# Kernel tuning notes

Measured on AMD Instinct MI355X. Metric: run time of the kernel, lower is better.

The kernel has to match this reference:

```python
import jax, jax.numpy as jnp
import numpy as np

B, C, H, W = 16, 256, 128, 128
RED = 16
RATES = (1, 2, 4)  # 1 + 4 + 16 = 21 pooled values per channel


def setup_inputs() -> dict:
    key = jax.random.key(0)
    ks = jax.random.split(key, 7)
    r = C // RED
    x = jax.random.normal(ks[0], (B, C, H, W), dtype=jnp.float32)
    # stacked per-channel fusion Linears: weight (C, 21), bias (C,)
    Wf = jax.random.normal(ks[1], (C, 21), dtype=jnp.float32) * 0.2
    bf = jax.random.normal(ks[2], (C,), dtype=jnp.float32) * 0.05
    # SE bottleneck FC (stored as (in, out) so y = x @ W + b)
    W1 = jax.random.normal(ks[3], (C, r), dtype=jnp.float32) * (1.0 / np.sqrt(C))
    b1 = jax.random.normal(ks[4], (r,), dtype=jnp.float32) * 0.05
    W2 = jax.random.normal(ks[5], (r, C), dtype=jnp.float32) * (1.0 / np.sqrt(r))
    b2 = jax.random.normal(ks[6], (C,), dtype=jnp.float32) * 0.05
    return {"x": x, "Wf": Wf, "bf": bf, "W1": W1, "b1": b1, "W2": W2, "b2": b2}


def _multiscale_pool(x):
    # kernel = stride = (H//rate, W//rate) -> output rate x rate, flattened
    b, c, h, w = x.shape
    outs = []
    for rate in RATES:
        ph, pw = h // rate, w // rate
        pooled = x.reshape(b, c, rate, ph, rate, pw).max(axis=(3, 5))  # (b,c,rate,rate)
        outs.append(pooled.reshape(b, c, rate * rate))
    return jnp.concatenate(outs, axis=2)  # (b, c, 21)


def reference(x, Wf, bf, W1, b1, W2, b2):
    p = _multiscale_pool(x)                              # (B, C, 21)
    fused = jnp.einsum('bcp,cp->bc', p, Wf) + bf         # per-channel 21->1 linears
    h = jax.nn.relu(fused @ W1 + b1)                      # SE squeeze
    s = h @ W2 + b2                                       # SE excite (NOTE: original forward applies NO sigmoid)
    return x * s[:, :, None, None]
```

## Files before the change

kernel.cpp:

```cpp
#include <hip/hip_runtime.h>

#define BB 16
#define CC 256
#define RR 16
#define HWPLANE 16384
#define NGROUPS 4
#define PLANES_PER_GROUP 1024

using f32x4 = __attribute__((ext_vector_type(4))) float;

__global__ __launch_bounds__(256) void pool_fuse_kernel(
    const float* __restrict__ x,
    const float* __restrict__ Wf,
    const float* __restrict__ bf,
    float* __restrict__ fused,
    int plane0)
{
    const int bc = plane0 + blockIdx.x;
    const int c  = bc & (CC - 1);
    const f32x4* xp = (const f32x4*)(x + (size_t)bc * HWPLANE);

    const int t    = threadIdx.x;
    const int lane = t & 63;
    const int wave = t >> 6;
    const int bx   = (t & 31) >> 3;

    __shared__ float wred[4][16];
    __shared__ float pb[16];

#pragma unroll
    for (int by = 0; by < 4; ++by) {
        float m = -3.402823466e+38f;
#pragma unroll
        for (int ii = 0; ii < 4; ++ii) {
            f32x4 v = xp[(by * 4 + ii) * 256 + t];
            m = fmaxf(m, fmaxf(fmaxf(v.x, v.y), fmaxf(v.z, v.w)));
        }
        m = fmaxf(m, __shfl_xor(m, 1));
        m = fmaxf(m, __shfl_xor(m, 2));
        m = fmaxf(m, __shfl_xor(m, 4));
        m = fmaxf(m, __shfl_xor(m, 32));
        if ((lane & 7) == 0 && lane < 32) wred[wave][by * 4 + bx] = m;
    }
    __syncthreads();

    if (t < 16)
        pb[t] = fmaxf(fmaxf(wred[0][t], wred[1][t]),
                      fmaxf(wred[2][t], wred[3][t]));
    __syncthreads();

    if (t == 0) {
        float q0 = fmaxf(fmaxf(pb[0],  pb[1]),  fmaxf(pb[4],  pb[5]));
        float q1 = fmaxf(fmaxf(pb[2],  pb[3]),  fmaxf(pb[6],  pb[7]));
        float q2 = fmaxf(fmaxf(pb[8],  pb[9]),  fmaxf(pb[12], pb[13]));
        float q3 = fmaxf(fmaxf(pb[10], pb[11]), fmaxf(pb[14], pb[15]));
        float g  = fmaxf(fmaxf(q0, q1), fmaxf(q2, q3));

        const float* w = Wf + c * 21;
        float acc = bf[c] + g * w[0]
                  + q0 * w[1] + q1 * w[2] + q2 * w[3] + q3 * w[4];
#pragma unroll
        for (int k = 0; k < 16; ++k) acc += pb[k] * w[5 + k];
        fused[bc] = acc;
    }
}

__global__ __launch_bounds__(256) void scale_se_kernel(
    const float* __restrict__ x,
    const float* __restrict__ W1,
    const float* __restrict__ b1,
    const float* __restrict__ W2,
    const float* __restrict__ b2,
    const float* __restrict__ fused,
    float* __restrict__ out,
    int plane0)
{
    const int bc = plane0 + blockIdx.x;
    const int b  = bc >> 8;
    const int c  = bc & (CC - 1);
    const int t  = threadIdx.x;

    __shared__ float hpart[16][16];
    __shared__ float hl[RR];
    __shared__ float svs;

    {
        const int j = t & 15, ch = t >> 4;
        float p = 0.f;
#pragma unroll
        for (int m = 0; m < 16; ++m) {
            const int cc = ch * 16 + m;
            p += fused[b * CC + cc] * W1[cc * RR + j];
        }
        hpart[ch][j] = p;
    }
    __syncthreads();
    if (t < RR) {
        float a = b1[t];
#pragma unroll
        for (int ch = 0; ch < 16; ++ch) a += hpart[ch][t];
        hl[t] = fmaxf(a, 0.f);
    }
    __syncthreads();
    if (t == 0) {
        float a = b2[c];
#pragma unroll
        for (int j = 0; j < RR; ++j) a += hl[j] * W2[j * CC + c];
        svs = a;
    }
    __syncthreads();

    const float sc = svs;
    const f32x4* xp = (const f32x4*)(x + (size_t)bc * HWPLANE);
    f32x4* op = (f32x4*)(out + (size_t)bc * HWPLANE);
#pragma unroll
    for (int i = 0; i < 16; ++i) {
        f32x4 v = xp[i * 256 + t];
        __builtin_nontemporal_store(v * sc, &op[i * 256 + t]);
    }
}

extern "C" void kernel_launch(void* const* d_in, const int* in_sizes, int n_in,
                              void* d_out, int out_size, void* d_ws, size_t ws_size,
                              hipStream_t stream) {
    const float* x  = (const float*)d_in[0];
    const float* Wf = (const float*)d_in[1];
    const float* bf = (const float*)d_in[2];
    const float* W1 = (const float*)d_in[3];
    const float* b1 = (const float*)d_in[4];
    const float* W2 = (const float*)d_in[5];
    const float* b2 = (const float*)d_in[6];
    float* out = (float*)d_out;

    float* fused = (float*)d_ws;

    for (int g = 0; g < NGROUPS; ++g) {
        const int plane0 = g * PLANES_PER_GROUP;
        pool_fuse_kernel<<<PLANES_PER_GROUP, 256, 0, stream>>>(
            x, Wf, bf, fused, plane0);
        scale_se_kernel<<<PLANES_PER_GROUP, 256, 0, stream>>>(
            x, W1, b1, W2, b2, fused, out, plane0);
    }
}
```

Baseline: 137.6 us.

## Software-pipeline pool and scale stages into one kernel per group

Merges the pooling and SE-scale kernels into one stage kernel. Each launch scales group g while pooling group g+1, which cuts the launch count from eight to five and lets the two stages overlap inside each launch. Each block now does both workloads one after the other, so it runs longer and streams two different planes. The L2 reuse of x between the pool and scale passes may drop because a plane is now pooled in one launch and scaled in the next.

```diff
diff --git a/kernel.cpp b/kernel.cpp
--- a/kernel.cpp
+++ b/kernel.cpp
@@ -9,114 +9,111 @@
 
 using f32x4 = __attribute__((ext_vector_type(4))) float;
 
-__global__ __launch_bounds__(256) void pool_fuse_kernel(
+__global__ __launch_bounds__(256) void spse_stage_kernel(
     const float* __restrict__ x,
     const float* __restrict__ Wf,
     const float* __restrict__ bf,
+    const float* __restrict__ W1,
+    const float* __restrict__ b1,
+    const float* __restrict__ W2,
+    const float* __restrict__ b2,
     float* __restrict__ fused,
-    int plane0)
+    float* __restrict__ out,
+    int scale_plane0,
+    int pool_plane0)
 {
-    const int bc = plane0 + blockIdx.x;
-    const int c  = bc & (CC - 1);
-    const f32x4* xp = (const f32x4*)(x + (size_t)bc * HWPLANE);
-
     const int t    = threadIdx.x;
     const int lane = t & 63;
     const int wave = t >> 6;
     const int bx   = (t & 31) >> 3;
 
+    __shared__ float hpart[16][16];
+    __shared__ float hl[RR];
+    __shared__ float svs;
     __shared__ float wred[4][16];
     __shared__ float pb[16];
 
+    if (scale_plane0 >= 0) {
+        const int bc = scale_plane0 + blockIdx.x;
+        const int b  = bc >> 8;
+        const int c  = bc & (CC - 1);
+
+        {
+            const int j = t & 15, ch = t >> 4;
+            float p = 0.f;
 #pragma unroll
-    for (int by = 0; by < 4; ++by) {
-        float m = -3.402823466e+38f;
+            for (int m = 0; m < 16; ++m) {
+                const int cc = ch * 16 + m;
+                p += fused[b * CC + cc] * W1[cc * RR + j];
+            }
+            hpart[ch][j] = p;
+        }
+        __syncthreads();
+        if (t < RR) {
+            float a = b1[t];
 #pragma unroll
-        for (int ii = 0; ii < 4; ++ii) {
-            f32x4 v = xp[(by * 4 + ii) * 256 + t];
-            m = fmaxf(m, fmaxf(fmaxf(v.x, v.y), fmaxf(v.z, v.w)));
+            for (int ch = 0; ch < 16; ++ch) a += hpart[ch][t];
+            hl[t] = fmaxf(a, 0.f);
         }
-        m = fmaxf(m, __shfl_xor(m, 1));
-        m = fmaxf(m, __shfl_xor(m, 2));
-        m = fmaxf(m, __shfl_xor(m, 4));
-        m = fmaxf(m, __shfl_xor(m, 32));
-        if ((lane & 7) == 0 && lane < 32) wred[wave][by * 4 + bx] = m;
+        __syncthreads();
+        if (t == 0) {
+            float a = b2[c];
+#pragma unroll
+            for (int j = 0; j < RR; ++j) a += hl[j] * W2[j * CC + c];
+            svs = a;
+        }
+        __syncthreads();
+
+        const float sc = svs;
+        const f32x4* xp = (const f32x4*)(x + (size_t)bc * HWPLANE);
+        f32x4* op = (f32x4*)(out + (size_t)bc * HWPLANE);
+#pragma unroll
+        for (int i = 0; i < 16; ++i) {
+            f32x4 v = xp[i * 256 + t];
+            __builtin_nontemporal_store(v * sc, &op[i * 256 + t]);
+        }
     }
-    __syncthreads();
 
-    if (t < 16)
-        pb[t] = fmaxf(fmaxf(wred[0][t], wred[1][t]),
-                      fmaxf(wred[2][t], wred[3][t]));
-    __syncthreads();
+    if (pool_plane0 >= 0) {
+        const int bc = pool_plane0 + blockIdx.x;
+        const int c  = bc & (CC - 1);
+        const f32x4* xp = (const f32x4*)(x + (size_t)bc * HWPLANE);
 
-    if (t == 0) {
-        float q0 = fmaxf(fmaxf(pb[0],  pb[1]),  fmaxf(pb[4],  pb[5]));
-        float q1 = fmaxf(fmaxf(pb[2],  pb[3]),  fmaxf(pb[6],  pb[7]));
-        float q2 = fmaxf(fmaxf(pb[8],  pb[9]),  fmaxf(pb[12], pb[13]));
-        float q3 = fmaxf(fmaxf(pb[10], pb[11]), fmaxf(pb[14], pb[15]));
-        float g  = fmaxf(fmaxf(q0, q1), fmaxf(q2, q3));
+#pragma unroll
+        for (int by = 0; by < 4; ++by) {
+            float m = -3.402823466e+38f;
+#pragma unroll
+            for (int ii = 0; ii < 4; ++ii) {
+                f32x4 v = xp[(by * 4 + ii) * 256 + t];
+                m = fmaxf(m, fmaxf(fmaxf(v.x, v.y), fmaxf(v.z, v.w)));
+            }
+            m = fmaxf(m, __shfl_xor(m, 1));
+            m = fmaxf(m, __shfl_xor(m, 2));
+            m = fmaxf(m, __shfl_xor(m, 4));
+            m = fmaxf(m, __shfl_xor(m, 32));
+            if ((lane & 7) == 0 && lane < 32) wred[wave][by * 4 + bx] = m;
+        }
+        __syncthreads();
 
-        const float* w = Wf + c * 21;
-        float acc = bf[c] + g * w[0]
-                  + q0 * w[1] + q1 * w[2] + q2 * w[3] + q3 * w[4];
+        if (t < 16)
+            pb[t] = fmaxf(fmaxf(wred[0][t], wred[1][t]),
+                          fmaxf(wred[2][t], wred[3][t]));
+        __syncthreads();
+
+        if (t == 0) {
+            float q0 = fmaxf(fmaxf(pb[0],  pb[1]),  fmaxf(pb[4],  pb[5]));
+            float q1 = fmaxf(fmaxf(pb[2],  pb[3]),  fmaxf(pb[6],  pb[7]));
+            float q2 = fmaxf(fmaxf(pb[8],  pb[9]),  fmaxf(pb[12], pb[13]));
+            float q3 = fmaxf(fmaxf(pb[10], pb[11]), fmaxf(pb[14], pb[15]));
+            float g  = fmaxf(fmaxf(q0, q1), fmaxf(q2, q3));
+
+            const float* w = Wf + c * 21;
+            float acc = bf[c] + g * w[0]
+                      + q0 * w[1] + q1 * w[2] + q2 * w[3] + q3 * w[4];
 #pragma unroll
-        for (int k = 0; k < 16; ++k) acc += pb[k] * w[5 + k];
-        fused[bc] = acc;
-    }
-}
-
-__global__ __launch_bounds__(256) void scale_se_kernel(
-    const float* __restrict__ x,
-    const float* __restrict__ W1,
-    const float* __restrict__ b1,
-    const float* __restrict__ W2,
-    const float* __restrict__ b2,
-    const float* __restrict__ fused,
-    float* __restrict__ out,
-    int plane0)
-{
-    const int bc = plane0 + blockIdx.x;
-    const int b  = bc >> 8;
-    const int c  = bc & (CC - 1);
-    const int t  = threadIdx.x;
-
-    __shared__ float hpart[16][16];
-    __shared__ float hl[RR];
-    __shared__ float svs;
-
-    {
-        const int j = t & 15, ch = t >> 4;
-        float p = 0.f;
-#pragma unroll
-        for (int m = 0; m < 16; ++m) {
-            const int cc = ch * 16 + m;
-            p += fused[b * CC + cc] * W1[cc * RR + j];
+            for (int k = 0; k < 16; ++k) acc += pb[k] * w[5 + k];
+            fused[bc] = acc;
         }
-        hpart[ch][j] = p;
-    }
-    __syncthreads();
-    if (t < RR) {
-        float a = b1[t];
-#pragma unroll
-        for (int ch = 0; ch < 16; ++ch) a += hpart[ch][t];
-        hl[t] = fmaxf(a, 0.f);
-    }
-    __syncthreads();
-    if (t == 0) {
-        float a = b2[c];
-#pragma unroll
-        for (int j = 0; j < RR; ++j) a += hl[j] * W2[j * CC + c];
-        svs = a;
-    }
-    __syncthreads();
-
-    const float sc = svs;
-    const f32x4* xp = (const f32x4*)(x + (size_t)bc * HWPLANE);
-    f32x4* op = (f32x4*)(out + (size_t)bc * HWPLANE);
-#pragma unroll
-    for (int i = 0; i < 16; ++i) {
-        f32x4 v = xp[i * 256 + t];
-        __builtin_nontemporal_store(v * sc, &op[i * 256 + t]);
     }
 }
 
@@ -134,11 +131,14 @@
 
     float* fused = (float*)d_ws;
 
-    for (int g = 0; g < NGROUPS; ++g) {
-        const int plane0 = g * PLANES_PER_GROUP;
-        pool_fuse_kernel<<<PLANES_PER_GROUP, 256, 0, stream>>>(
-            x, Wf, bf, fused, plane0);
-        scale_se_kernel<<<PLANES_PER_GROUP, 256, 0, stream>>>(
-            x, W1, b1, W2, b2, fused, out, plane0);
+    spse_stage_kernel<<<PLANES_PER_GROUP, 256, 0, stream>>>(
+        x, Wf, bf, W1, b1, W2, b2, fused, out, -1, 0);
+    for (int g = 0; g < NGROUPS - 1; ++g) {
+        spse_stage_kernel<<<PLANES_PER_GROUP, 256, 0, stream>>>(
+            x, Wf, bf, W1, b1, W2, b2, fused, out,
+            g * PLANES_PER_GROUP, (g + 1) * PLANES_PER_GROUP);
     }
+    spse_stage_kernel<<<PLANES_PER_GROUP, 256, 0, stream>>>(
+        x, Wf, bf, W1, b1, W2, b2, fused, out,
+        (NGROUPS - 1) * PLANES_PER_GROUP, -1);
 }
```

Result: no change. 135.6 us (-1.5%).

## Fuse pool and scale into persistent kernel with register-held planes and cohort barriers

Applied to the files above, without the earlier changes.

Replaces the eight alternating pool/scale launches with one persistent kernel of 512 blocks. Each block keeps its 64KB plane in registers across the pooling and scaling phases, so x is read from memory once instead of twice. Blocks handling the same batch sync through atomic-counter cohort barriers before computing the SE vector. This relies on all 512 blocks being co-resident, otherwise it deadlocks. It also adds register pressure and barrier spin latency at each of the eight stages.

```diff
diff --git a/kernel.cpp b/kernel.cpp
--- a/kernel.cpp
+++ b/kernel.cpp
@@ -4,119 +4,140 @@
 #define CC 256
 #define RR 16
 #define HWPLANE 16384
-#define NGROUPS 4
-#define PLANES_PER_GROUP 1024
+#define NBLOCKS 512
+#define NSTAGES 8
+#define PLANES_PER_STAGE 512
+#define COHORT 256
 
 using f32x4 = __attribute__((ext_vector_type(4))) float;
 
-__global__ __launch_bounds__(256) void pool_fuse_kernel(
+__global__ void init_kernel(unsigned* bar) {
+    if (threadIdx.x < 16) bar[threadIdx.x] = 0u;
+}
+
+__device__ __forceinline__ void cohort_barrier(unsigned* cnt) {
+    __syncthreads();
+    if (threadIdx.x == 0) {
+        __hip_atomic_fetch_add(cnt, 1u, __ATOMIC_RELEASE,
+                               __HIP_MEMORY_SCOPE_AGENT);
+        unsigned v;
+        do {
+            __builtin_amdgcn_s_sleep(8);
+            v = __hip_atomic_load(cnt, __ATOMIC_RELAXED,
+                                  __HIP_MEMORY_SCOPE_AGENT);
+        } while (v < COHORT);
+    }
+    __syncthreads();
+}
+
+__global__ __launch_bounds__(256) void spse_persist_kernel(
     const float* __restrict__ x,
     const float* __restrict__ Wf,
     const float* __restrict__ bf,
-    float* __restrict__ fused,
-    int plane0)
+    const float* __restrict__ W1,
+    const float* __restrict__ b1,
+    const float* __restrict__ W2,
+    const float* __restrict__ b2,
+    float* __restrict__ out,
+    unsigned* __restrict__ bar,
+    float* __restrict__ fused)
 {
-    const int bc = plane0 + blockIdx.x;
-    const int c  = bc & (CC - 1);
-    const f32x4* xp = (const f32x4*)(x + (size_t)bc * HWPLANE);
-
     const int t    = threadIdx.x;
     const int lane = t & 63;
     const int wave = t >> 6;
     const int bx   = (t & 31) >> 3;
+    const int blk  = blockIdx.x;
 
     __shared__ float wred[4][16];
     __shared__ float pb[16];
-
-#pragma unroll
-    for (int by = 0; by < 4; ++by) {
-        float m = -3.402823466e+38f;
-#pragma unroll
-        for (int ii = 0; ii < 4; ++ii) {
-            f32x4 v = xp[(by * 4 + ii) * 256 + t];
-            m = fmaxf(m, fmaxf(fmaxf(v.x, v.y), fmaxf(v.z, v.w)));
-        }
-        m = fmaxf(m, __shfl_xor(m, 1));
-        m = fmaxf(m, __shfl_xor(m, 2));
-        m = fmaxf(m, __shfl_xor(m, 4));
-        m = fmaxf(m, __shfl_xor(m, 32));
-        if ((lane & 7) == 0 && lane < 32) wred[wave][by * 4 + bx] = m;
-    }
-    __syncthreads();
-
-    if (t < 16)
-        pb[t] = fmaxf(fmaxf(wred[0][t], wred[1][t]),
-                      fmaxf(wred[2][t], wred[3][t]));
-    __syncthreads();
-
-    if (t == 0) {
-        float q0 = fmaxf(fmaxf(pb[0],  pb[1]),  fmaxf(pb[4],  pb[5]));
-        float q1 = fmaxf(fmaxf(pb[2],  pb[3]),  fmaxf(pb[6],  pb[7]));
-        float q2 = fmaxf(fmaxf(pb[8],  pb[9]),  fmaxf(pb[12], pb[13]));
-        float q3 = fmaxf(fmaxf(pb[10], pb[11]), fmaxf(pb[14], pb[15]));
-        float g  = fmaxf(fmaxf(q0, q1), fmaxf(q2, q3));
-
-        const float* w = Wf + c * 21;
-        float acc = bf[c] + g * w[0]
-                  + q0 * w[1] + q1 * w[2] + q2 * w[3] + q3 * w[4];
-#pragma unroll
-        for (int k = 0; k < 16; ++k) acc += pb[k] * w[5 + k];
-        fused[bc] = acc;
-    }
-}
-
-__global__ __launch_bounds__(256) void scale_se_kernel(
-    const float* __restrict__ x,
-    const float* __restrict__ W1,
-    const float* __restrict__ b1,
-    const float* __restrict__ W2,
-    const float* __restrict__ b2,
-    const float* __restrict__ fused,
-    float* __restrict__ out,
-    int plane0)
-{
-    const int bc = plane0 + blockIdx.x;
-    const int b  = bc >> 8;
-    const int c  = bc & (CC - 1);
-    const int t  = threadIdx.x;
-
+    __shared__ float fl[CC];
     __shared__ float hpart[16][16];
     __shared__ float hl[RR];
     __shared__ float svs;
 
-    {
-        const int j = t & 15, ch = t >> 4;
-        float p = 0.f;
+    for (int s = 0; s < NSTAGES; ++s) {
+        const int bc = s * PLANES_PER_STAGE + blk;
+        const int b  = bc >> 8;
+        const int c  = bc & (CC - 1);
+        const f32x4* xp = (const f32x4*)(x + (size_t)bc * HWPLANE);
+        f32x4* op = (f32x4*)(out + (size_t)bc * HWPLANE);
+
+        f32x4 v[16];
 #pragma unroll
-        for (int m = 0; m < 16; ++m) {
-            const int cc = ch * 16 + m;
-            p += fused[b * CC + cc] * W1[cc * RR + j];
+        for (int i = 0; i < 16; ++i)
+            v[i] = __builtin_nontemporal_load(&xp[i * 256 + t]);
+
+#pragma unroll
+        for (int by = 0; by < 4; ++by) {
+            float m = -3.402823466e+38f;
+#pragma unroll
+            for (int ii = 0; ii < 4; ++ii) {
+                f32x4 w4 = v[by * 4 + ii];
+                m = fmaxf(m, fmaxf(fmaxf(w4.x, w4.y), fmaxf(w4.z, w4.w)));
+            }
+            m = fmaxf(m, __shfl_xor(m, 1));
+            m = fmaxf(m, __shfl_xor(m, 2));
+            m = fmaxf(m, __shfl_xor(m, 4));
+            m = fmaxf(m, __shfl_xor(m, 32));
+            if ((lane & 7) == 0 && lane < 32) wred[wave][by * 4 + bx] = m;
         }
-        hpart[ch][j] = p;
-    }
-    __syncthreads();
-    if (t < RR) {
-        float a = b1[t];
+        __syncthreads();
+        if (t < 16)
+            pb[t] = fmaxf(fmaxf(wred[0][t], wred[1][t]),
+                          fmaxf(wred[2][t], wred[3][t]));
+        __syncthreads();
+
+        if (t == 0) {
+            float q0 = fmaxf(fmaxf(pb[0],  pb[1]),  fmaxf(pb[4],  pb[5]));
+            float q1 = fmaxf(fmaxf(pb[2],  pb[3]),  fmaxf(pb[6],  pb[7]));
+            float q2 = fmaxf(fmaxf(pb[8],  pb[9]),  fmaxf(pb[12], pb[13]));
+            float q3 = fmaxf(fmaxf(pb[10], pb[11]), fmaxf(pb[14], pb[15]));
+            float g  = fmaxf(fmaxf(q0, q1), fmaxf(q2, q3));
+            const float* w = Wf + c * 21;
+            float acc = bf[c] + g * w[0]
+                      + q0 * w[1] + q1 * w[2] + q2 * w[3] + q3 * w[4];
 #pragma unroll
-        for (int ch = 0; ch < 16; ++ch) a += hpart[ch][t];
-        hl[t] = fmaxf(a, 0.f);
-    }
-    __syncthreads();
-    if (t == 0) {
-        float a = b2[c];
+            for (int k = 0; k < 16; ++k) acc += pb[k] * w[5 + k];
+            __hip_atomic_store(&fused[bc], acc, __ATOMIC_RELAXED,
+                               __HIP_MEMORY_SCOPE_AGENT);
+        }
+
+        cohort_barrier(&bar[s * 2 + (blk >> 8)]);
+
+        fl[t] = __hip_atomic_load(&fused[b * CC + t], __ATOMIC_RELAXED,
+                                  __HIP_MEMORY_SCOPE_AGENT);
+        __syncthreads();
+
+        {
+            const int j = t & 15, ch = t >> 4;
+            float p = 0.f;
 #pragma unroll
-        for (int j = 0; j < RR; ++j) a += hl[j] * W2[j * CC + c];
-        svs = a;
-    }
-    __syncthreads();
+            for (int m = 0; m < 16; ++m)
+                p += fl[ch * 16 + m] * W1[(ch * 16 + m) * RR + j];
+            hpart[ch][j] = p;
+        }
+        __syncthreads();
+        if (t < RR) {
+            float a = b1[t];
+#pragma unroll
+            for (int ch = 0; ch < 16; ++ch) a += hpart[ch][t];
+            hl[t] = fmaxf(a, 0.f);
+        }
+        __syncthreads();
+        if (t == 0) {
+            float a = b2[c];
+#pragma unroll
+            for (int j = 0; j < RR; ++j) a += hl[j] * W2[j * CC + c];
+            svs = a;
+        }
+        __syncthreads();
 
-    const float sc = svs;
-    const f32x4* xp = (const f32x4*)(x + (size_t)bc * HWPLANE);
-    f32x4* op = (f32x4*)(out + (size_t)bc * HWPLANE);
+        const float sc = svs;
 #pragma unroll
-    for (int i = 0; i < 16; ++i) {
-        f32x4 v = xp[i * 256 + t];
-        __builtin_nontemporal_store(v * sc, &op[i * 256 + t]);
+        for (int i = 0; i < 16; ++i)
+            __builtin_nontemporal_store(v[i] * sc, &op[i * 256 + t]);
+
+        __syncthreads();
     }
 }
 
@@ -132,13 +153,10 @@
     const float* b2 = (const float*)d_in[6];
     float* out = (float*)d_out;
 
-    float* fused = (float*)d_ws;
+    unsigned* bar = (unsigned*)d_ws;
+    float* fused  = (float*)((char*)d_ws + 256);
 
-    for (int g = 0; g < NGROUPS; ++g) {
-        const int plane0 = g * PLANES_PER_GROUP;
-        pool_fuse_kernel<<<PLANES_PER_GROUP, 256, 0, stream>>>(
-            x, Wf, bf, fused, plane0);
-        scale_se_kernel<<<PLANES_PER_GROUP, 256, 0, stream>>>(
-            x, W1, b1, W2, b2, fused, out, plane0);
-    }
+    init_kernel<<<1, 64, 0, stream>>>(bar);
+    spse_persist_kernel<<<NBLOCKS, 256, 0, stream>>>(
+        x, Wf, bf, W1, b1, W2, b2, out, bar, fused);
 }
```

Result: slower. 378.0 us (+174.7%).
